# Kernel optimization log

Hardware: AMD Instinct MI355X
Metric: run time of the kernel (lower is better)

## Reference

```python
import jax, jax.numpy as jnp
import numpy as np


def setup_inputs() -> dict:
    key = jax.random.key(0)
    k1, k2 = jax.random.split(key)
    B, L, D = 8, 4096, 64
    x = jax.random.normal(k1, (B, L, D), dtype=jnp.float32)
    # per-token validity mask [B, L, 1] with 0/1 entries (outer product builds the pairwise mask)
    mask = jax.random.randint(k2, (B, L, 1), 0, 2, dtype=jnp.int32)
    return {"x": x, "mask": mask}


def reference(x, mask):
    # OriAttention with head=1: q = k = v = x, shapes [B, L, D]
    B, L, D = x.shape
    scale = D ** 0.25  # note: fourth root of d, as in the original
    scores = jnp.einsum('bqd,bkd->bqk', x, x) / scale  # [B, L, L]
    # pairwise mask via outer product of the [B, L, 1] token mask, then bool cast
    mf = mask.astype(jnp.float32)
    pair = jnp.matmul(mf, mf.transpose(0, 2, 1)) != 0.0  # [B, L, L] bool
    scores = jnp.where(pair, scores, jnp.float32(-10000000.0))
    # original softmaxes along dim=2 of [B, H, Lq, Lk], i.e. over the QUERY axis
    attn = jax.nn.softmax(scores, axis=1)  # normalize over q for each k
    # then transposes (2,3) and matmuls with v: out[b,k,:] = sum_q attn[b,q,k] * v[b,q,:]
    out = jnp.einsum('bqk,bqd->bkd', attn, x)  # [B, L, D]
    return out
```

## Files before the change

kernel.cpp:

```cpp
#include <hip/hip_runtime.h>
#include <stdint.h>

typedef __attribute__((ext_vector_type(8))) __bf16 bf16x8;
typedef __attribute__((ext_vector_type(4))) __bf16 bf16x4;
typedef __attribute__((ext_vector_type(4))) float f32x4;

#define MFMA_BF16(A, B, C) __builtin_amdgcn_mfma_f32_16x16x32_bf16((A), (B), (C), 0, 0, 0)
#define VBAR() asm volatile("s_waitcnt vmcnt(0) lgkmcnt(0)\ns_barrier" ::: "memory")

__device__ __forceinline__ void gload16(const void* g, void* l) {
  __builtin_amdgcn_global_load_lds((const __attribute__((address_space(1))) void*)g,
                                   (__attribute__((address_space(3))) void*)l, 16, 0, 0);
}

namespace {

constexpr int kBatch = 8;
constexpr int kL = 4096;
constexpr int kD = 64;
constexpr int kQB = 128;
constexpr int kKB = 64;
constexpr int kSlotPad = 4096;
constexpr int kMaxTiles = 64;
constexpr int kSlotCap = 2304;
constexpr int kSplits = 4;
constexpr float kC = 1.4426950408889634f / 2.8284271247461903f;

constexpr size_t kWsPartialOff = 0;
constexpr size_t kWsCountOff = 65536;
constexpr size_t kWsRankOff = 131136;
constexpr size_t kWsPlOff = 196672;
constexpr size_t kWsXchOff = 1376320;
constexpr size_t kWsVtgOff = 5570624;
constexpr size_t kWsPaccOff = 9764928;

__device__ __forceinline__ int fk(int r) { return (r & 3) | ((r >> 1) & 4); }

__device__ __forceinline__ size_t slotrow(int s, int b, int slot, bool fb) {
  return fb ? ((size_t)b * kL + slot) : ((size_t)(s * kBatch + b) * kSlotCap + slot);
}

__device__ __forceinline__ float bf16hi_f(uint32_t u) { return __uint_as_float(u << 16); }

__global__ __launch_bounds__(256) void k_prep(const float* __restrict__ x,
                                              const int* __restrict__ mask,
                                              float* __restrict__ partial,
                                              uint16_t* __restrict__ rank,
                                              int* __restrict__ counts,
                                              __bf16* __restrict__ xch,
                                              __bf16* __restrict__ vtg) {
  const int b = blockIdx.y;
  const int bx = blockIdx.x;
  const int t = threadIdx.x;

  if (bx >= 64) {
    const int part = bx - 64;
    __shared__ float sm[256];
    const int d = t & 63, rs = t >> 6;
    const float* xb = x + (size_t)b * kL * kD;
    float s = 0.0f;
    const int r0 = part * 128 + rs;
    for (int i = 0; i < 32; ++i) s += xb[(size_t)(r0 + i * 4) * kD + d];
    sm[t] = s;
    __syncthreads();
    if (t < 64)
      partial[(b * 32 + part) * 64 + t] = sm[t] + sm[t + 64] + sm[t + 128] + sm[t + 192];
    return;
  }

  __shared__ int scan[256];
  __shared__ int slotTab[64];
  __shared__ __align__(16) __bf16 tmp[kKB][80];

  const int* mb = mask + b * kL;
  const int r0 = t * 16;
  int msk16 = 0, cnt = 0;
#pragma unroll
  for (int i = 0; i < 16; ++i) {
    if (mb[r0 + i] != 0) { msk16 |= 1 << i; ++cnt; }
  }
  scan[t] = cnt;
  if (t < 64) slotTab[t] = -1;
  __syncthreads();
#pragma unroll
  for (int off = 1; off < 256; off <<= 1) {
    const int v = (t >= off) ? scan[t - off] : 0;
    __syncthreads();
    scan[t] += v;
    __syncthreads();
  }
  const int count = scan[255];
  const int base = bx * 64;
  {
    int rk = scan[t] - cnt;
#pragma unroll
    for (int i = 0; i < 16; ++i) {
      if (msk16 & (1 << i)) {
        if (rk >= base && rk < base + 64) slotTab[rk - base] = r0 + i;
        ++rk;
      }
    }
  }
  if (bx == 0) {
    int rk = scan[t] - cnt;
#pragma unroll
    for (int i = 0; i < 16; ++i) {
      if (msk16 & (1 << i)) { rank[b * kL + r0 + i] = (uint16_t)rk; ++rk; }
    }
    if (t == 0) counts[b] = count;
  }
  __syncthreads();

  const int NT = (count + kKB - 1) >> 6;
  if (bx >= NT) return;

  const int srow = t >> 2, q3 = t & 3;
  const int slot = base + srow;
  const int rowi = slotTab[srow];
  float v16[16];
  if (rowi >= 0) {
    const float4* p = (const float4*)(x + ((size_t)b * kL + rowi) * kD + q3 * 16);
    const float4 a0 = p[0], a1 = p[1], a2 = p[2], a3 = p[3];
    v16[0] = a0.x; v16[1] = a0.y; v16[2] = a0.z; v16[3] = a0.w;
    v16[4] = a1.x; v16[5] = a1.y; v16[6] = a1.z; v16[7] = a1.w;
    v16[8] = a2.x; v16[9] = a2.y; v16[10] = a2.z; v16[11] = a2.w;
    v16[12] = a3.x; v16[13] = a3.y; v16[14] = a3.z; v16[15] = a3.w;
  } else {
#pragma unroll
    for (int i = 0; i < 16; ++i) v16[i] = 0.0f;
  }
  bf16x8 u0, u1;
#pragma unroll
  for (int j = 0; j < 8; ++j) { u0[j] = (__bf16)v16[j]; u1[j] = (__bf16)v16[8 + j]; }

  {
    __bf16* xrow = xch + ((size_t)b * kSlotPad + slot) * kD;
    const int f = fk(srow);
    *(bf16x8*)(xrow + (((2 * q3) ^ f) << 3)) = u0;
    *(bf16x8*)(xrow + (((2 * q3 + 1) ^ f) << 3)) = u1;
  }
  *(bf16x8*)&tmp[srow][q3 * 16] = u0;
  *(bf16x8*)&tmp[srow][q3 * 16 + 8] = u1;
  __syncthreads();
  {
    const int d = t >> 2, kq = t & 3;
    bf16x8 c0, c1;
#pragma unroll
    for (int i = 0; i < 8; ++i) {
      c0[i] = tmp[kq * 16 + i][d];
      c1[i] = tmp[kq * 16 + 8 + i][d];
    }
    __bf16* vrow = vtg + (((size_t)b * kMaxTiles + bx) * kKB + d) * kD;
    const int e = d & 7;
    *(bf16x8*)(vrow + (((2 * kq) ^ e) << 3)) = c0;
    *(bf16x8*)(vrow + (((2 * kq + 1) ^ e) << 3)) = c1;
  }
}

__global__ __launch_bounds__(256, 4) void k_attn(const __bf16* __restrict__ xch,
                                                 const __bf16* __restrict__ vtg,
                                                 const int* __restrict__ counts,
                                                 float* __restrict__ pl,
                                                 __bf16* __restrict__ pacc) {
  const int b = blockIdx.x;
  const int s = blockIdx.y;
  const int qt = blockIdx.z;

  int cmax = 0;
#pragma unroll
  for (int i = 0; i < kBatch; ++i) cmax = max(cmax, counts[i]);
  const bool fb = cmax > kSlotCap;
  const int nS = fb ? 1 : (int)gridDim.y;
  if (fb && s > 0) return;

  const int count = counts[b];
  if (qt * kQB >= count) return;
  const int NTtot = (count + kKB - 1) >> 6;
  const int TPS = (NTtot + nS - 1) / nS;
  const int t0 = s * TPS;
  const int t1 = min(NTtot, t0 + TPS);

  const int tid = threadIdx.x;
  const int wave = tid >> 6;
  const int lane = tid & 63;
  const int lg = lane >> 4;
  const int lr = lane & 15;

  int qpos[2];
  bool qvalid[2];
  size_t sr[2];
#pragma unroll
  for (int h = 0; h < 2; ++h) {
    qpos[h] = qt * kQB + h * 64 + wave * 16 + lr;
    qvalid[h] = qpos[h] < count;
    sr[h] = slotrow(s, b, qpos[h], fb);
  }

  if (t0 >= t1) {
#pragma unroll
    for (int h = 0; h < 2; ++h) {
      if (qvalid[h]) {
        const bf16x4 z = (bf16x4)(__bf16)0.0f;
#pragma unroll
        for (int dt = 0; dt < 4; ++dt) *(bf16x4*)&pacc[sr[h] * kD + dt * 16 + lg * 4] = z;
        if (lg == 0) pl[sr[h]] = 0.0f;
      }
    }
    return;
  }

  const __bf16* __restrict__ xb = xch + (size_t)b * kSlotPad * kD;
  const __bf16* __restrict__ vb = vtg + (size_t)b * kMaxTiles * (kKB * kD);

  __shared__ __align__(16) __bf16 KhB[2][kKB * kD];
  __shared__ __align__(16) __bf16 VtB[2][kKB * kD];

  bf16x8 qh[2][2];
#pragma unroll
  for (int h = 0; h < 2; ++h) {
    const int qr = qvalid[h] ? qpos[h] : 0;
    const __bf16* qrow = xb + (size_t)qr * kD;
    const int f = fk(qr & 63);
#pragma unroll
    for (int kt = 0; kt < 2; ++kt)
      qh[h][kt] = *(const bf16x8*)(qrow + (((kt * 4 + lg) ^ f) << 3));
  }

  f32x4 acc[2][4];
  f32x4 acc_l[2];
#pragma unroll
  for (int h = 0; h < 2; ++h) {
#pragma unroll
    for (int i = 0; i < 4; ++i) acc[h][i] = (f32x4)0.0f;
    acc_l[h] = (f32x4)0.0f;
  }

  bf16x8 vone;
#pragma unroll
  for (int j = 0; j < 8; ++j) vone[j] = (lr == 0) ? (__bf16)1.0f : (__bf16)0.0f;

  auto stage = [&](int t, int buf) {
    const size_t goff = (size_t)t * (kKB * kD);
    const int lo = lane * 8;
#pragma unroll
    for (int c = 0; c < 2; ++c) {
      const int eo = wave * 1024 + c * 512;
      gload16(xb + goff + eo + lo, &KhB[buf][eo]);
      gload16(vb + goff + eo + lo, &VtB[buf][eo]);
    }
  };

  stage(t0, 0);
  VBAR();

  int cur = 0;
  for (int t = t0; t < t1; ++t) {
    const bool havenext = (t + 1 < t1);
    if (havenext) stage(t + 1, cur ^ 1);

    const __bf16* Kh = &KhB[cur][0];
    const __bf16* Vt = &VtB[cur][0];

    f32x4 S_[2][2][2];
    __builtin_amdgcn_s_setprio(1);
#pragma unroll
    for (int g = 0; g < 2; ++g) {
#pragma unroll
      for (int tt = 0; tt < 2; ++tt) {
        const int krow = g * 32 + ((lr >> 2) << 3) + tt * 4 + (lr & 3);
        const int f = fk(krow);
        f32x4 s0 = (f32x4)0.0f, s1 = (f32x4)0.0f;
#pragma unroll
        for (int kt = 0; kt < 2; ++kt) {
          const bf16x8 ah = *(const bf16x8*)&Kh[(krow << 6) + (((kt * 4 + lg) ^ f) << 3)];
          s0 = MFMA_BF16(ah, qh[0][kt], s0);
          s1 = MFMA_BF16(ah, qh[1][kt], s1);
        }
        S_[0][g][tt] = s0;
        S_[1][g][tt] = s1;
      }
    }
    __builtin_amdgcn_s_setprio(0);

    float p[2][2][2][4];
#pragma unroll
    for (int h = 0; h < 2; ++h)
#pragma unroll
      for (int g = 0; g < 2; ++g)
#pragma unroll
        for (int tt = 0; tt < 2; ++tt)
#pragma unroll
          for (int r = 0; r < 4; ++r)
            p[h][g][tt][r] = __builtin_amdgcn_exp2f(S_[h][g][tt][r] * kC);

    if (t == NTtot - 1 && (count & 63)) {
      const int valid = count & 63;
#pragma unroll
      for (int h = 0; h < 2; ++h)
#pragma unroll
        for (int g = 0; g < 2; ++g)
#pragma unroll
          for (int tt = 0; tt < 2; ++tt)
#pragma unroll
            for (int r = 0; r < 4; ++r) {
              const int kl2 = g * 32 + lg * 8 + tt * 4 + r;
              if (kl2 >= valid) p[h][g][tt][r] = 0.0f;
            }
    }

    bf16x8 pf[2][2];
#pragma unroll
    for (int h = 0; h < 2; ++h)
#pragma unroll
      for (int g = 0; g < 2; ++g)
#pragma unroll
        for (int tt = 0; tt < 2; ++tt)
#pragma unroll
          for (int r = 0; r < 4; ++r) pf[h][g][tt * 4 + r] = (__bf16)p[h][g][tt][r];

    __builtin_amdgcn_s_setprio(1);
#pragma unroll
    for (int g = 0; g < 2; ++g) {
      acc_l[0] = MFMA_BF16(vone, pf[0][g], acc_l[0]);
      acc_l[1] = MFMA_BF16(vone, pf[1][g], acc_l[1]);
#pragma unroll
      for (int dt = 0; dt < 4; ++dt) {
        const int d = dt * 16 + lr;
        const bf16x8 vf =
            *(const bf16x8*)&Vt[(d << 6) + ((((g << 2) + lg) ^ (d & 7)) << 3)];
        acc[0][dt] = MFMA_BF16(vf, pf[0][g], acc[0][dt]);
        acc[1][dt] = MFMA_BF16(vf, pf[1][g], acc[1][dt]);
      }
    }
    __builtin_amdgcn_s_setprio(0);

    if (havenext) VBAR();
    cur ^= 1;
  }

#pragma unroll
  for (int h = 0; h < 2; ++h) {
    if (qvalid[h]) {
#pragma unroll
      for (int dt = 0; dt < 4; ++dt) {
        bf16x4 v;
#pragma unroll
        for (int r = 0; r < 4; ++r) v[r] = (__bf16)acc[h][dt][r];
        *(bf16x4*)&pacc[sr[h] * kD + dt * 16 + lg * 4] = v;
      }
      if (lg == 0) pl[sr[h]] = acc_l[h][0];
    }
  }
}

template <int TS>
__global__ __launch_bounds__(256) void k_post(const int* __restrict__ mask,
                                              const float* __restrict__ partial,
                                              const uint16_t* __restrict__ rank,
                                              const int* __restrict__ counts,
                                              const float* __restrict__ pl,
                                              const __bf16* __restrict__ pacc,
                                              float* __restrict__ out) {
  const int b = blockIdx.y;
  const int c = blockIdx.x;
  const int t = threadIdx.x;

  int cmax = 0;
#pragma unroll
  for (int i = 0; i < kBatch; ++i) cmax = max(cmax, counts[i]);
  const bool fb = cmax > kSlotCap;

  __shared__ float mean[64];
  __shared__ float winv[32];
  __shared__ int slotL[32];

  if (t < 64) {
    float s = 0.0f;
    for (int p = 0; p < 32; ++p) s += partial[(b * 32 + p) * 64 + t];
    mean[t] = s * (1.0f / (float)kL);
  } else if (t < 96) {
    const int i = t - 64;
    const int r = c * 32 + i;
    if (mask[b * kL + r] == 0) {
      slotL[i] = -1;
    } else {
      const int slot = rank[b * kL + r];
      slotL[i] = slot;
      float L = 0.0f;
      if (!fb) {
#pragma unroll
        for (int s2 = 0; s2 < TS; ++s2)
          L += pl[(size_t)(s2 * kBatch + b) * kSlotCap + slot];
      } else {
        L = pl[(size_t)b * kL + slot];
      }
      winv[i] = 1.0f / L;
    }
  }
  __syncthreads();

  const int d0 = (t & 31) * 2;
  const int rg = t >> 5;
#pragma unroll
  for (int it = 0; it < 4; ++it) {
    const int rl = it * 8 + rg;
    const int slot = slotL[rl];
    float o0, o1;
    if (slot < 0) {
      o0 = mean[d0];
      o1 = mean[d0 + 1];
    } else if (!fb) {
      o0 = 0.0f;
      o1 = 0.0f;
#pragma unroll
      for (int s2 = 0; s2 < TS; ++s2) {
        const uint32_t v = *(const uint32_t*)&pacc[((size_t)(s2 * kBatch + b) * kSlotCap +
                                                    slot) * kD + d0];
        o0 += bf16hi_f(v & 0xFFFFu);
        o1 += bf16hi_f(v >> 16);
      }
      o0 *= winv[rl];
      o1 *= winv[rl];
    } else {
      const uint32_t v = *(const uint32_t*)&pacc[((size_t)b * kL + slot) * kD + d0];
      o0 = winv[rl] * bf16hi_f(v & 0xFFFFu);
      o1 = winv[rl] * bf16hi_f(v >> 16);
    }
    *(float2*)&out[((size_t)b * kL + c * 32 + rl) * kD + d0] = float2{o0, o1};
  }
}

}

extern "C" void kernel_launch(void* const* d_in, const int* in_sizes, int n_in,
                              void* d_out, int out_size, void* d_ws, size_t ws_size,
                              hipStream_t stream) {
  const float* x = (const float*)d_in[0];
  const int* mask = (const int*)d_in[1];
  float* out = (float*)d_out;
  char* ws = (char*)d_ws;
  float* partial = (float*)(ws + kWsPartialOff);
  int* counts = (int*)(ws + kWsCountOff);
  uint16_t* rank = (uint16_t*)(ws + kWsRankOff);
  float* pl = (float*)(ws + kWsPlOff);
  __bf16* xch = (__bf16*)(ws + kWsXchOff);
  __bf16* vtg = (__bf16*)(ws + kWsVtgOff);
  __bf16* pacc = (__bf16*)(ws + kWsPaccOff);

  int S = kSplits;
  while (S > 1 && ws_size < kWsPaccOff + (size_t)S * kBatch * kSlotCap * kD * 2) S >>= 1;

  k_prep<<<dim3(96, kBatch), dim3(256), 0, stream>>>(x, mask, partial, rank, counts,
                                                     xch, vtg);
  k_attn<<<dim3(kBatch, S, kL / kQB), dim3(256), 0, stream>>>(xch, vtg, counts, pl, pacc);
  switch (S) {
    case 4:
      k_post<4><<<dim3(128, kBatch), dim3(256), 0, stream>>>(mask, partial, rank, counts,
                                                             pl, pacc, out);
      break;
    case 2:
      k_post<2><<<dim3(128, kBatch), dim3(256), 0, stream>>>(mask, partial, rank, counts,
                                                             pl, pacc, out);
      break;
    default:
      k_post<1><<<dim3(128, kBatch), dim3(256), 0, stream>>>(mask, partial, rank, counts,
                                                             pl, pacc, out);
      break;
  }
}
```

Measured before the change: 37.93 us.

## Double query block per workgroup and double key splits to reuse K/V tiles

Each attention workgroup now covers 256 queries instead of 128, with four 16-query groups per wave. Every K/V tile staged in LDS therefore feeds twice as many MFMAs, which cuts LDS staging and global K/V traffic per query. The key dimension is split 8 ways instead of 4, so the grid stays the same size, and a k_post<8> instantiation is added to merge the extra partials. The inner loop now handles one 32-key half at a time to hold down register use, but the kernel still allows only 2 workgroups per SIMD instead of 4. That lowers occupancy and doubles the partial-result traffic that k_post must reduce.

```diff
diff --git a/kernel.cpp b/kernel.cpp
--- a/kernel.cpp
+++ b/kernel.cpp
@@ -18,12 +18,12 @@
 constexpr int kBatch = 8;
 constexpr int kL = 4096;
 constexpr int kD = 64;
-constexpr int kQB = 128;
+constexpr int kQB = 256;
 constexpr int kKB = 64;
 constexpr int kSlotPad = 4096;
 constexpr int kMaxTiles = 64;
 constexpr int kSlotCap = 2304;
-constexpr int kSplits = 4;
+constexpr int kSplits = 8;
 constexpr float kC = 1.4426950408889634f / 2.8284271247461903f;
 
 constexpr size_t kWsPartialOff = 0;
@@ -157,7 +157,7 @@
   }
 }
 
-__global__ __launch_bounds__(256, 4) void k_attn(const __bf16* __restrict__ xch,
+__global__ __launch_bounds__(256, 2) void k_attn(const __bf16* __restrict__ xch,
                                                  const __bf16* __restrict__ vtg,
                                                  const int* __restrict__ counts,
                                                  float* __restrict__ pl,
@@ -186,11 +186,11 @@
   const int lg = lane >> 4;
   const int lr = lane & 15;
 
-  int qpos[2];
-  bool qvalid[2];
-  size_t sr[2];
-#pragma unroll
-  for (int h = 0; h < 2; ++h) {
+  int qpos[4];
+  bool qvalid[4];
+  size_t sr[4];
+#pragma unroll
+  for (int h = 0; h < 4; ++h) {
     qpos[h] = qt * kQB + h * 64 + wave * 16 + lr;
     qvalid[h] = qpos[h] < count;
     sr[h] = slotrow(s, b, qpos[h], fb);
@@ -198,7 +198,7 @@
 
   if (t0 >= t1) {
 #pragma unroll
-    for (int h = 0; h < 2; ++h) {
+    for (int h = 0; h < 4; ++h) {
       if (qvalid[h]) {
         const bf16x4 z = (bf16x4)(__bf16)0.0f;
 #pragma unroll
@@ -215,9 +215,9 @@
   __shared__ __align__(16) __bf16 KhB[2][kKB * kD];
   __shared__ __align__(16) __bf16 VtB[2][kKB * kD];
 
-  bf16x8 qh[2][2];
-#pragma unroll
-  for (int h = 0; h < 2; ++h) {
+  bf16x8 qh[4][2];
+#pragma unroll
+  for (int h = 0; h < 4; ++h) {
     const int qr = qvalid[h] ? qpos[h] : 0;
     const __bf16* qrow = xb + (size_t)qr * kD;
     const int f = fk(qr & 63);
@@ -226,10 +226,10 @@
       qh[h][kt] = *(const bf16x8*)(qrow + (((kt * 4 + lg) ^ f) << 3));
   }
 
-  f32x4 acc[2][4];
-  f32x4 acc_l[2];
-#pragma unroll
-  for (int h = 0; h < 2; ++h) {
+  f32x4 acc[4][4];
+  f32x4 acc_l[4];
+#pragma unroll
+  for (int h = 0; h < 4; ++h) {
 #pragma unroll
     for (int i = 0; i < 4; ++i) acc[h][i] = (f32x4)0.0f;
     acc_l[h] = (f32x4)0.0f;
@@ -261,85 +261,74 @@
     const __bf16* Kh = &KhB[cur][0];
     const __bf16* Vt = &VtB[cur][0];
 
-    f32x4 S_[2][2][2];
-    __builtin_amdgcn_s_setprio(1);
+    const bool tail = (t == NTtot - 1) && (count & 63);
+    const int valid = count & 63;
+
 #pragma unroll
     for (int g = 0; g < 2; ++g) {
+      f32x4 S_[4][2];
+      __builtin_amdgcn_s_setprio(1);
 #pragma unroll
       for (int tt = 0; tt < 2; ++tt) {
         const int krow = g * 32 + ((lr >> 2) << 3) + tt * 4 + (lr & 3);
         const int f = fk(krow);
-        f32x4 s0 = (f32x4)0.0f, s1 = (f32x4)0.0f;
+        f32x4 s0 = (f32x4)0.0f, s1 = (f32x4)0.0f, s2 = (f32x4)0.0f, s3 = (f32x4)0.0f;
 #pragma unroll
         for (int kt = 0; kt < 2; ++kt) {
           const bf16x8 ah = *(const bf16x8*)&Kh[(krow << 6) + (((kt * 4 + lg) ^ f) << 3)];
           s0 = MFMA_BF16(ah, qh[0][kt], s0);
           s1 = MFMA_BF16(ah, qh[1][kt], s1);
+          s2 = MFMA_BF16(ah, qh[2][kt], s2);
+          s3 = MFMA_BF16(ah, qh[3][kt], s3);
         }
-        S_[0][g][tt] = s0;
-        S_[1][g][tt] = s1;
-      }
-    }
-    __builtin_amdgcn_s_setprio(0);
-
-    float p[2][2][2][4];
-#pragma unroll
-    for (int h = 0; h < 2; ++h)
-#pragma unroll
-      for (int g = 0; g < 2; ++g)
-#pragma unroll
-        for (int tt = 0; tt < 2; ++tt)
-#pragma unroll
-          for (int r = 0; r < 4; ++r)
-            p[h][g][tt][r] = __builtin_amdgcn_exp2f(S_[h][g][tt][r] * kC);
-
-    if (t == NTtot - 1 && (count & 63)) {
-      const int valid = count & 63;
-#pragma unroll
-      for (int h = 0; h < 2; ++h)
-#pragma unroll
-        for (int g = 0; g < 2; ++g)
-#pragma unroll
-          for (int tt = 0; tt < 2; ++tt)
-#pragma unroll
-            for (int r = 0; r < 4; ++r) {
+        S_[0][tt] = s0;
+        S_[1][tt] = s1;
+        S_[2][tt] = s2;
+        S_[3][tt] = s3;
+      }
+      __builtin_amdgcn_s_setprio(0);
+
+      bf16x8 pf[4];
+#pragma unroll
+      for (int h = 0; h < 4; ++h) {
+#pragma unroll
+        for (int tt = 0; tt < 2; ++tt) {
+#pragma unroll
+          for (int r = 0; r < 4; ++r) {
+            float pv = __builtin_amdgcn_exp2f(S_[h][tt][r] * kC);
+            if (tail) {
               const int kl2 = g * 32 + lg * 8 + tt * 4 + r;
-              if (kl2 >= valid) p[h][g][tt][r] = 0.0f;
+              if (kl2 >= valid) pv = 0.0f;
             }
-    }
-
-    bf16x8 pf[2][2];
-#pragma unroll
-    for (int h = 0; h < 2; ++h)
-#pragma unroll
-      for (int g = 0; g < 2; ++g)
-#pragma unroll
-        for (int tt = 0; tt < 2; ++tt)
-#pragma unroll
-          for (int r = 0; r < 4; ++r) pf[h][g][tt * 4 + r] = (__bf16)p[h][g][tt][r];
-
-    __builtin_amdgcn_s_setprio(1);
-#pragma unroll
-    for (int g = 0; g < 2; ++g) {
-      acc_l[0] = MFMA_BF16(vone, pf[0][g], acc_l[0]);
-      acc_l[1] = MFMA_BF16(vone, pf[1][g], acc_l[1]);
+            pf[h][tt * 4 + r] = (__bf16)pv;
+          }
+        }
+      }
+
+      __builtin_amdgcn_s_setprio(1);
+      acc_l[0] = MFMA_BF16(vone, pf[0], acc_l[0]);
+      acc_l[1] = MFMA_BF16(vone, pf[1], acc_l[1]);
+      acc_l[2] = MFMA_BF16(vone, pf[2], acc_l[2]);
+      acc_l[3] = MFMA_BF16(vone, pf[3], acc_l[3]);
 #pragma unroll
       for (int dt = 0; dt < 4; ++dt) {
         const int d = dt * 16 + lr;
         const bf16x8 vf =
             *(const bf16x8*)&Vt[(d << 6) + ((((g << 2) + lg) ^ (d & 7)) << 3)];
-        acc[0][dt] = MFMA_BF16(vf, pf[0][g], acc[0][dt]);
-        acc[1][dt] = MFMA_BF16(vf, pf[1][g], acc[1][dt]);
-      }
-    }
-    __builtin_amdgcn_s_setprio(0);
+        acc[0][dt] = MFMA_BF16(vf, pf[0], acc[0][dt]);
+        acc[1][dt] = MFMA_BF16(vf, pf[1], acc[1][dt]);
+        acc[2][dt] = MFMA_BF16(vf, pf[2], acc[2][dt]);
+        acc[3][dt] = MFMA_BF16(vf, pf[3], acc[3][dt]);
+      }
+      __builtin_amdgcn_s_setprio(0);
+    }
 
     if (havenext) VBAR();
     cur ^= 1;
   }
 
 #pragma unroll
-  for (int h = 0; h < 2; ++h) {
+  for (int h = 0; h < 4; ++h) {
     if (qvalid[h]) {
 #pragma unroll
       for (int dt = 0; dt < 4; ++dt) {
@@ -454,6 +443,10 @@
                                                      xch, vtg);
   k_attn<<<dim3(kBatch, S, kL / kQB), dim3(256), 0, stream>>>(xch, vtg, counts, pl, pacc);
   switch (S) {
+    case 8:
+      k_post<8><<<dim3(128, kBatch), dim3(256), 0, stream>>>(mask, partial, rank, counts,
+                                                             pl, pacc, out);
+      break;
     case 4:
       k_post<4><<<dim3(128, kBatch), dim3(256), 0, stream>>>(mask, partial, rank, counts,
                                                              pl, pacc, out);
```

Result: slower. 45.93 us (+21.1%).
